# Performance work log

Measured on AMD Instinct MI355X. Metric: run time of the kernel, lower is better.

## Reference

```python
import jax, jax.numpy as jnp
import numpy as np

NEG_BIG = -9.0e15  # matches torch's -9000000000000000.0
LEAKY_SLOPE = 0.01  # nn.LeakyReLU default


def setup_inputs() -> dict:
    key = jax.random.key(0)
    k1, k2, k3, k4, k5, k6 = jax.random.split(key, 6)
    B, N, NEMB, NHID = 1, 8192, 128, 64
    x = jax.random.normal(k1, (B, N, NEMB), dtype=jnp.float32)
    adj = jax.random.randint(k2, (B, N, N), 0, 2, dtype=jnp.int32)
    # learned parameters (xavier-ish scale)
    w_weight = jax.random.normal(k3, (NHID, NEMB), dtype=jnp.float32) * (1.0 / np.sqrt(NEMB))
    w_bias = jnp.zeros((NHID,), dtype=jnp.float32)
    a_weight = jax.random.normal(k4, (1, 2 * NHID), dtype=jnp.float32) * (1.0 / np.sqrt(2 * NHID))
    a_bias = jnp.zeros((1,), dtype=jnp.float32)
    return {"x": x, "adj": adj, "w_weight": w_weight, "w_bias": w_bias,
            "a_weight": a_weight, "a_bias": a_bias}


def reference(x, adj, w_weight, w_bias, a_weight, a_bias):
    # h = W x + b : [B, N, F]
    h = jnp.einsum("bnd,fd->bnf", x, w_weight) + w_bias
    F = h.shape[-1]
    # The torch code forms a[b,i,j] = concat(h_i, h_j) then Linear(2F->1).
    # Equivalent decomposition avoids the [B,N,N,2F] tensor:
    # e[b,i,j] = leaky_relu(h_i . a_src + h_j . a_dst + a_bias)
    a_src, a_dst = a_weight[0, :F], a_weight[0, F:]
    s_src = jnp.einsum("bnf,f->bn", h, a_src)  # [B, N]
    s_dst = jnp.einsum("bnf,f->bn", h, a_dst)  # [B, N]
    e = jax.nn.leaky_relu(s_src[:, :, None] + s_dst[:, None, :] + a_bias[0],
                          negative_slope=LEAKY_SLOPE)  # [B, N, N]
    # masked_scatter_ semantics: True positions (row-major over the WHOLE
    # flattened tensor) receive e's elements taken sequentially in order.
    mask_flat = (adj > 0).reshape(-1)
    take_idx = jnp.cumsum(mask_flat.astype(jnp.int32)) - 1  # position in source stream
    src_flat = e.reshape(-1)
    att = jnp.where(mask_flat, src_flat[take_idx], jnp.float32(NEG_BIG)).reshape(e.shape)
    # softmax over dim=2, dropout in eval mode (identity)
    att = jax.nn.softmax(att, axis=2)
    out = jax.nn.elu(jnp.einsum("bij,bjf->bif", att, h))  # [B, N, F]
    return out
```

## Files before the change

kernel.cpp:

```cpp
#include <hip/hip_runtime.h>
#include <hip/hip_bf16.h>
#include <cstdint>
#include <cstddef>

#define N 8192
#define F 64
#define NEMB 128
#define BI 16
#define BJ 256
#define NWRD (N/16)
#define LEAKY 0.01f

typedef __attribute__((ext_vector_type(8))) short bf16x8;
typedef __attribute__((ext_vector_type(4))) float f32x4;

__device__ __forceinline__ float wave_reduce_sum_f(float v){
  #pragma unroll
  for (int d = 32; d > 0; d >>= 1) v += __shfl_xor(v, d, 64);
  return v;
}
__device__ __forceinline__ int wave_reduce_sum_i(int v){
  #pragma unroll
  for (int d = 32; d > 0; d >>= 1) v += __shfl_xor(v, d, 64);
  return v;
}
__device__ __forceinline__ int wave_incl_scan_i(int v, int lane){
  #pragma unroll
  for (int d = 1; d < 64; d <<= 1){
    int u = __shfl_up(v, d, 64);
    if (lane >= d) v += u;
  }
  return v;
}
__device__ __forceinline__ unsigned short f2bf(float x){
  union { float f; unsigned u; } v; v.f = x;
  unsigned r = v.u + 0x7fff + ((v.u >> 16) & 1);
  return (unsigned short)(r >> 16);
}

extern "C" __global__ void __launch_bounds__(256)
k_h(const float* __restrict__ x, const float* __restrict__ ww, const float* __restrict__ wb,
    const float* __restrict__ aw, float* __restrict__ h,
    float* __restrict__ ssrc, float* __restrict__ sdst){
  __shared__ float xs[4][NEMB];
  const int t = threadIdx.x, w = t >> 6, lane = t & 63;
  const int n0 = blockIdx.x * 4;
  ((float2*)&xs[0][0])[t] = ((const float2*)(x + (size_t)n0 * NEMB))[t];
  __syncthreads();
  const int n = n0 + w;
  const float4* w4 = (const float4*)(ww + (size_t)lane * NEMB);
  const float4* x4 = (const float4*)&xs[w][0];
  float acc = wb[lane];
  #pragma unroll
  for (int k = 0; k < NEMB/4; ++k){
    float4 a = x4[k]; float4 b = w4[k];
    acc = fmaf(a.x, b.x, acc);
    acc = fmaf(a.y, b.y, acc);
    acc = fmaf(a.z, b.z, acc);
    acc = fmaf(a.w, b.w, acc);
  }
  h[(size_t)n * F + lane] = acc;
  float vs = wave_reduce_sum_f(acc * aw[lane]);
  float vd = wave_reduce_sum_f(acc * aw[F + lane]);
  if (lane == 0){ ssrc[n] = vs; sdst[n] = vd; }
}

extern "C" __global__ void __launch_bounds__(256)
k_tr(const float* __restrict__ h, unsigned short* __restrict__ ht){
  __shared__ float tile[64][65];
  const int t = threadIdx.x;
  const int n0 = blockIdx.x * 64;
  #pragma unroll
  for (int s = 0; s < 4; ++s){
    const int r = s*16 + (t>>4);
    const int c = (t&15)*4;
    const float4 v = *(const float4*)(h + (size_t)(n0+r)*F + c);
    tile[r][c] = v.x; tile[r][c+1] = v.y; tile[r][c+2] = v.z; tile[r][c+3] = v.w;
  }
  __syncthreads();
  const int f = t >> 2, jq = t & 3;
  unsigned short buf[16];
  #pragma unroll
  for (int k = 0; k < 16; ++k) buf[k] = f2bf(tile[jq*16 + k][f]);
  *(uint4*)(ht + (size_t)f*N + n0 + jq*16)     = *(uint4*)&buf[0];
  *(uint4*)(ht + (size_t)f*N + n0 + jq*16 + 8) = *(uint4*)&buf[8];
}

extern "C" __global__ void __launch_bounds__(256)
k_pack(const int* __restrict__ adj, unsigned short* __restrict__ bm, int* __restrict__ cnt){
  const int i = blockIdx.x, t = threadIdx.x;
  int total = 0;
  #pragma unroll
  for (int half = 0; half < 2; ++half){
    const int jb = half*4096 + t*16;
    const int4* p4 = (const int4*)(adj + (size_t)i*N + jb);
    unsigned m = 0;
    #pragma unroll
    for (int k = 0; k < 4; ++k){
      int4 a = p4[k];
      m |= (unsigned)(a.x > 0) << (k*4+0);
      m |= (unsigned)(a.y > 0) << (k*4+1);
      m |= (unsigned)(a.z > 0) << (k*4+2);
      m |= (unsigned)(a.w > 0) << (k*4+3);
    }
    bm[(size_t)i*NWRD + (jb>>4)] = (unsigned short)m;
    total += __popc(m);
  }
  total = wave_reduce_sum_i(total);
  __shared__ int ws_[4];
  if ((t & 63) == 0) ws_[t >> 6] = total;
  __syncthreads();
  if (t == 0) cnt[i] = ws_[0] + ws_[1] + ws_[2] + ws_[3];
}

extern "C" __global__ void __launch_bounds__(1024)
k_scan(const int* __restrict__ cnt, int* __restrict__ base){
  __shared__ int wsum[16];
  const int t = threadIdx.x, lane = t & 63, w = t >> 6;
  int4 aa = ((const int4*)cnt)[t * 2];
  int4 bb = ((const int4*)cnt)[t * 2 + 1];
  int v[8] = {aa.x, aa.y, aa.z, aa.w, bb.x, bb.y, bb.z, bb.w};
  int local = 0;
  #pragma unroll
  for (int k = 0; k < 8; ++k){ int tmp = v[k]; v[k] = local; local += tmp; }
  int inc = wave_incl_scan_i(local, lane);
  int wexcl = inc - local;
  if (lane == 63) wsum[w] = inc;
  __syncthreads();
  if (t == 0){
    int run = 0;
    #pragma unroll
    for (int k = 0; k < 16; ++k){ int tmp = wsum[k]; wsum[k] = run; run += tmp; }
  }
  __syncthreads();
  const int b0 = wsum[w] + wexcl;
  ((int4*)base)[t * 2]     = make_int4(b0 + v[0], b0 + v[1], b0 + v[2], b0 + v[3]);
  ((int4*)base)[t * 2 + 1] = make_int4(b0 + v[4], b0 + v[5], b0 + v[6], b0 + v[7]);
}

extern "C" __global__ void __launch_bounds__(256, 3)
k_main(const unsigned short* __restrict__ bm, const unsigned short* __restrict__ ht,
       const float* __restrict__ ssrc, const float* __restrict__ sdst,
       const float* __restrict__ abias, const int* __restrict__ base,
       float* __restrict__ out){
  __shared__ __attribute__((aligned(16))) char ht_lds[64*512];
  __shared__ __attribute__((aligned(16))) char pt_lds[16*512];
  __shared__ float denom_lds[BI];
  const int t = threadIdx.x, w = t >> 6, lane = t & 63;
  const int i0 = blockIdx.x * BI;
  const int r = t >> 4, g = t & 15;
  const float ab = abias[0];
  int rank = base[i0 + r];
  float dsum = 0.f;
  f32x4 acc = {0.f, 0.f, 0.f, 0.f};

  const int fr = lane & 15, ks = lane >> 4;
  const int fB = w*16 + fr;
  const char* aBase = pt_lds + fr*512;
  const char* bBase = ht_lds + fB*512;
  const int sA = (fr & 7) << 4;
  const int sB = (fB & 7) << 4;

  for (int j0 = 0; j0 < N; j0 += BJ){
    __syncthreads();
    #pragma unroll
    for (int k = 0; k < 8; ++k){
      const int L = (w*8 + k) * 1024;
      const int f = (w*8 + k) * 2 + (lane >> 5);
      const int b = (lane & 31) * 16;
      const char* src = (const char*)ht + (size_t)f*(N*2) + j0*2 + (b ^ ((f & 7) << 4));
      __builtin_amdgcn_global_load_lds((const __attribute__((address_space(1))) void*)src,
                                       (__attribute__((address_space(3))) void*)(ht_lds + L),
                                       16, 0, 0);
    }
    {
      const unsigned m = bm[(size_t)(i0 + r)*NWRD + (j0 >> 4) + g];
      const int c = __popc(m);
      int inc = c;
      #pragma unroll
      for (int d = 1; d < 16; d <<= 1){
        int u = __shfl_up(inc, d, 16);
        if (g >= d) inc += u;
      }
      const int rowtot = __shfl(inc, 15, 16);
      int q = rank + inc - c;
      rank += rowtot;
      unsigned pk[8];
      #pragma unroll
      for (int bb = 0; bb < 16; ++bb){
        float p = 0.f;
        if ((m >> bb) & 1u){
          float e = ssrc[q >> 13] + sdst[q & (N - 1)] + ab;
          e = (e > 0.f) ? e : LEAKY * e;
          p = __expf(e);
          dsum += p;
          ++q;
        }
        if (bb & 1) pk[bb >> 1] |= (unsigned)f2bf(p) << 16;
        else        pk[bb >> 1]  = (unsigned)f2bf(p);
      }
      char* pb = pt_lds + r*512;
      const int sw = (r & 7) << 4;
      *(uint4*)(pb + ((g*32)      ^ sw)) = make_uint4(pk[0], pk[1], pk[2], pk[3]);
      *(uint4*)(pb + ((g*32 + 16) ^ sw)) = make_uint4(pk[4], pk[5], pk[6], pk[7]);
    }
    __syncthreads();
    #pragma unroll
    for (int kk = 0; kk < 8; ++kk){
      const int off = kk*64 + ks*16;
      bf16x8 av = *(const bf16x8*)(aBase + (off ^ sA));
      bf16x8 bv = *(const bf16x8*)(bBase + (off ^ sB));
      acc = __builtin_amdgcn_mfma_f32_16x16x32_bf16(av, bv, acc, 0, 0, 0);
    }
  }
  #pragma unroll
  for (int d = 8; d > 0; d >>= 1) dsum += __shfl_xor(dsum, d, 16);
  if (g == 0) denom_lds[r] = dsum;
  __syncthreads();
  #pragma unroll
  for (int reg = 0; reg < 4; ++reg){
    const int il = ks*4 + reg;
    const float dn = denom_lds[il];
    float v = (dn > 0.f) ? acc[reg] / dn : 0.f;
    const float o = (v > 0.f) ? v : (__expf(v) - 1.f);
    out[(size_t)(i0 + il)*F + w*16 + fr] = o;
  }
}

extern "C" void kernel_launch(void* const* d_in, const int* in_sizes, int n_in,
                              void* d_out, int out_size, void* d_ws, size_t ws_size,
                              hipStream_t stream){
  const float* x   = (const float*)d_in[0];
  const int*   adj = (const int*)d_in[1];
  const float* ww  = (const float*)d_in[2];
  const float* wb  = (const float*)d_in[3];
  const float* aw  = (const float*)d_in[4];
  const float* ab  = (const float*)d_in[5];
  float* out = (float*)d_out;

  char* ws = (char*)d_ws;
  float*          h    = (float*)(ws);
  unsigned short* ht   = (unsigned short*)(ws + (size_t)N*F*4);
  float*          ssrc = (float*)(ws + (size_t)N*F*4 + (size_t)N*F*2);
  float*          sdst = ssrc + N;
  int*            cnt  = (int*)(sdst + N);
  int*            base = cnt + N;
  unsigned short* bm   = (unsigned short*)(base + N);

  k_h   <<<N/4,  256, 0, stream>>>(x, ww, wb, aw, h, ssrc, sdst);
  k_tr  <<<N/64, 256, 0, stream>>>(h, ht);
  k_pack<<<N,    256, 0, stream>>>(adj, bm, cnt);
  k_scan<<<1,   1024, 0, stream>>>(cnt, base);
  k_main<<<N/BI, 256, 0, stream>>>(bm, ht, ssrc, sdst, ab, base, out);
}
```

Baseline: 187.5 us.

## Fuse adjacency packing and prefix scan into main kernel via decoupled lookback

Removes the separate pack and scan kernels. Each main block now takes a dynamic ticket, packs its 16 adjacency rows into an LDS bitmask, and computes its global rank offset with a single-pass decoupled-lookback scan over per-block partials. The per-bit rank inside the inner loop is now computed with popcount instead of a serial increment. This cuts two launches and the round trip of the bitmask through global memory. In exchange LDS use rises, the occupancy hint drops from 3 to 2 blocks, and blocks serialize on the lookback spin.

```diff
diff --git a/kernel.cpp b/kernel.cpp
--- a/kernel.cpp
+++ b/kernel.cpp
@@ -8,7 +8,7 @@
 #define NEMB 128
 #define BI 16
 #define BJ 256
-#define NWRD (N/16)
+#define NBLK (N/BI)
 #define LEAKY 0.01f
 
 typedef __attribute__((ext_vector_type(8))) short bf16x8;
@@ -22,14 +22,6 @@
 __device__ __forceinline__ int wave_reduce_sum_i(int v){
   #pragma unroll
   for (int d = 32; d > 0; d >>= 1) v += __shfl_xor(v, d, 64);
-  return v;
-}
-__device__ __forceinline__ int wave_incl_scan_i(int v, int lane){
-  #pragma unroll
-  for (int d = 1; d < 64; d <<= 1){
-    int u = __shfl_up(v, d, 64);
-    if (lane >= d) v += u;
-  }
   return v;
 }
 __device__ __forceinline__ unsigned short f2bf(float x){
@@ -41,9 +33,14 @@
 extern "C" __global__ void __launch_bounds__(256)
 k_h(const float* __restrict__ x, const float* __restrict__ ww, const float* __restrict__ wb,
     const float* __restrict__ aw, float* __restrict__ h,
-    float* __restrict__ ssrc, float* __restrict__ sdst){
+    float* __restrict__ ssrc, float* __restrict__ sdst,
+    unsigned* __restrict__ partials, int* __restrict__ ticket){
+  const int t = threadIdx.x, w = t >> 6, lane = t & 63;
+  if (blockIdx.x == 0){
+    partials[t] = 0; partials[t + 256] = 0;
+    if (t == 0) *ticket = 0;
+  }
   __shared__ float xs[4][NEMB];
-  const int t = threadIdx.x, w = t >> 6, lane = t & 63;
   const int n0 = blockIdx.x * 4;
   ((float2*)&xs[0][0])[t] = ((const float2*)(x + (size_t)n0 * NEMB))[t];
   __syncthreads();
@@ -86,71 +83,76 @@
   *(uint4*)(ht + (size_t)f*N + n0 + jq*16 + 8) = *(uint4*)&buf[8];
 }
 
-extern "C" __global__ void __launch_bounds__(256)
-k_pack(const int* __restrict__ adj, unsigned short* __restrict__ bm, int* __restrict__ cnt){
-  const int i = blockIdx.x, t = threadIdx.x;
-  int total = 0;
-  #pragma unroll
-  for (int half = 0; half < 2; ++half){
-    const int jb = half*4096 + t*16;
-    const int4* p4 = (const int4*)(adj + (size_t)i*N + jb);
-    unsigned m = 0;
-    #pragma unroll
-    for (int k = 0; k < 4; ++k){
-      int4 a = p4[k];
-      m |= (unsigned)(a.x > 0) << (k*4+0);
-      m |= (unsigned)(a.y > 0) << (k*4+1);
-      m |= (unsigned)(a.z > 0) << (k*4+2);
-      m |= (unsigned)(a.w > 0) << (k*4+3);
-    }
-    bm[(size_t)i*NWRD + (jb>>4)] = (unsigned short)m;
-    total += __popc(m);
-  }
-  total = wave_reduce_sum_i(total);
-  __shared__ int ws_[4];
-  if ((t & 63) == 0) ws_[t >> 6] = total;
-  __syncthreads();
-  if (t == 0) cnt[i] = ws_[0] + ws_[1] + ws_[2] + ws_[3];
-}
-
-extern "C" __global__ void __launch_bounds__(1024)
-k_scan(const int* __restrict__ cnt, int* __restrict__ base){
-  __shared__ int wsum[16];
-  const int t = threadIdx.x, lane = t & 63, w = t >> 6;
-  int4 aa = ((const int4*)cnt)[t * 2];
-  int4 bb = ((const int4*)cnt)[t * 2 + 1];
-  int v[8] = {aa.x, aa.y, aa.z, aa.w, bb.x, bb.y, bb.z, bb.w};
-  int local = 0;
-  #pragma unroll
-  for (int k = 0; k < 8; ++k){ int tmp = v[k]; v[k] = local; local += tmp; }
-  int inc = wave_incl_scan_i(local, lane);
-  int wexcl = inc - local;
-  if (lane == 63) wsum[w] = inc;
-  __syncthreads();
+extern "C" __global__ void __launch_bounds__(256, 2)
+k_main(const int* __restrict__ adj, const unsigned short* __restrict__ ht,
+       const float* __restrict__ ssrc, const float* __restrict__ sdst,
+       const float* __restrict__ abias,
+       unsigned* __restrict__ partials, int* __restrict__ ticket,
+       float* __restrict__ out){
+  __shared__ __attribute__((aligned(16))) char ht_lds[64*512];
+  __shared__ __attribute__((aligned(16))) char pt_lds[16*512];
+  __shared__ unsigned short bm_lds[BI][N/16];
+  __shared__ float denom_lds[BI];
+  __shared__ int cnt_lds[BI];
+  __shared__ int base_lds[BI];
+  __shared__ int vid_s, gbase_s;
+
+  const int t = threadIdx.x, w = t >> 6, lane = t & 63;
+  if (t == 0) vid_s = atomicAdd(ticket, 1);
+  __syncthreads();
+  const int vid = vid_s;
+  const int i0 = vid * BI;
+
+  #pragma unroll
+  for (int rr = 0; rr < 4; ++rr){
+    const int i = i0 + w*4 + rr;
+    const int4* row4 = (const int4*)(adj + (size_t)i * N);
+    int rcnt = 0;
+    #pragma unroll 4
+    for (int it = 0; it < 32; ++it){
+      const int4 a = row4[it*64 + lane];
+      unsigned nib = (unsigned)(a.x>0) | ((unsigned)(a.y>0)<<1) |
+                     ((unsigned)(a.z>0)<<2) | ((unsigned)(a.w>0)<<3);
+      rcnt += __popc(nib);
+      unsigned word = nib << ((lane & 3) * 4);
+      word |= __shfl_xor(word, 1, 64);
+      word |= __shfl_xor(word, 2, 64);
+      if ((lane & 3) == 0) bm_lds[w*4+rr][it*16 + (lane>>2)] = (unsigned short)word;
+    }
+    rcnt = wave_reduce_sum_i(rcnt);
+    if (lane == 0) cnt_lds[w*4+rr] = rcnt;
+  }
+  __syncthreads();
+
   if (t == 0){
     int run = 0;
     #pragma unroll
-    for (int k = 0; k < 16; ++k){ int tmp = wsum[k]; wsum[k] = run; run += tmp; }
-  }
-  __syncthreads();
-  const int b0 = wsum[w] + wexcl;
-  ((int4*)base)[t * 2]     = make_int4(b0 + v[0], b0 + v[1], b0 + v[2], b0 + v[3]);
-  ((int4*)base)[t * 2 + 1] = make_int4(b0 + v[4], b0 + v[5], b0 + v[6], b0 + v[7]);
-}
-
-extern "C" __global__ void __launch_bounds__(256, 3)
-k_main(const unsigned short* __restrict__ bm, const unsigned short* __restrict__ ht,
-       const float* __restrict__ ssrc, const float* __restrict__ sdst,
-       const float* __restrict__ abias, const int* __restrict__ base,
-       float* __restrict__ out){
-  __shared__ __attribute__((aligned(16))) char ht_lds[64*512];
-  __shared__ __attribute__((aligned(16))) char pt_lds[16*512];
-  __shared__ float denom_lds[BI];
-  const int t = threadIdx.x, w = t >> 6, lane = t & 63;
-  const int i0 = blockIdx.x * BI;
+    for (int k = 0; k < BI; ++k){ int c = cnt_lds[k]; base_lds[k] = run; run += c; }
+    const unsigned pub = ((unsigned)run << 2) | (vid == 0 ? 2u : 1u);
+    __hip_atomic_store(&partials[vid], pub, __ATOMIC_RELEASE, __HIP_MEMORY_SCOPE_AGENT);
+    unsigned long long excl = 0;
+    if (vid > 0){
+      int look = vid - 1;
+      while (1){
+        unsigned v;
+        do {
+          v = __hip_atomic_load(&partials[look], __ATOMIC_ACQUIRE, __HIP_MEMORY_SCOPE_AGENT);
+        } while (!(v & 3u));
+        excl += (v >> 2);
+        if ((v & 3u) == 2u) break;
+        --look;
+      }
+      __hip_atomic_store(&partials[vid],
+                         (unsigned)(((excl + (unsigned long long)(unsigned)run) << 2) | 2u),
+                         __ATOMIC_RELEASE, __HIP_MEMORY_SCOPE_AGENT);
+    }
+    gbase_s = (int)excl;
+  }
+  __syncthreads();
+
   const int r = t >> 4, g = t & 15;
   const float ab = abias[0];
-  int rank = base[i0 + r];
+  int rank = gbase_s + base_lds[r];
   float dsum = 0.f;
   f32x4 acc = {0.f, 0.f, 0.f, 0.f};
 
@@ -174,7 +176,7 @@
                                        16, 0, 0);
     }
     {
-      const unsigned m = bm[(size_t)(i0 + r)*NWRD + (j0 >> 4) + g];
+      const unsigned m = bm_lds[r][(j0 >> 4) + g];
       const int c = __popc(m);
       int inc = c;
       #pragma unroll
@@ -183,18 +185,18 @@
         if (g >= d) inc += u;
       }
       const int rowtot = __shfl(inc, 15, 16);
-      int q = rank + inc - c;
+      const int q0 = rank + inc - c;
       rank += rowtot;
       unsigned pk[8];
       #pragma unroll
       for (int bb = 0; bb < 16; ++bb){
         float p = 0.f;
         if ((m >> bb) & 1u){
-          float e = ssrc[q >> 13] + sdst[q & (N - 1)] + ab;
+          const int qb = q0 + __popc(m & ((1u << bb) - 1u));
+          float e = ssrc[qb >> 13] + sdst[qb & (N - 1)] + ab;
           e = (e > 0.f) ? e : LEAKY * e;
           p = __expf(e);
           dsum += p;
-          ++q;
         }
         if (bb & 1) pk[bb >> 1] |= (unsigned)f2bf(p) << 16;
         else        pk[bb >> 1]  = (unsigned)f2bf(p);
@@ -239,17 +241,14 @@
   float* out = (float*)d_out;
 
   char* ws = (char*)d_ws;
-  float*          h    = (float*)(ws);
-  unsigned short* ht   = (unsigned short*)(ws + (size_t)N*F*4);
-  float*          ssrc = (float*)(ws + (size_t)N*F*4 + (size_t)N*F*2);
-  float*          sdst = ssrc + N;
-  int*            cnt  = (int*)(sdst + N);
-  int*            base = cnt + N;
-  unsigned short* bm   = (unsigned short*)(base + N);
-
-  k_h   <<<N/4,  256, 0, stream>>>(x, ww, wb, aw, h, ssrc, sdst);
+  float*          h        = (float*)(ws);
+  unsigned short* ht       = (unsigned short*)(ws + (size_t)N*F*4);
+  float*          ssrc     = (float*)(ws + (size_t)N*F*4 + (size_t)N*F*2);
+  float*          sdst     = ssrc + N;
+  unsigned*       partials = (unsigned*)(sdst + N);
+  int*            ticket   = (int*)(partials + NBLK);
+
+  k_h   <<<N/4,  256, 0, stream>>>(x, ww, wb, aw, h, ssrc, sdst, partials, ticket);
   k_tr  <<<N/64, 256, 0, stream>>>(h, ht);
-  k_pack<<<N,    256, 0, stream>>>(adj, bm, cnt);
-  k_scan<<<1,   1024, 0, stream>>>(cnt, base);
-  k_main<<<N/BI, 256, 0, stream>>>(bm, ht, ssrc, sdst, ab, base, out);
-}
+  k_main<<<NBLK, 256, 0, stream>>>(adj, ht, ssrc, sdst, ab, partials, ticket, out);
+}
```

After: 360.5 us. 1.92x slower.

## Split attention rows across two blocks, double-buffer P tiles, and stream sdst contiguously

Applied to the files above, without the earlier changes.

The main kernel now splits each 16-row group's j-range into two halves handled by separate blocks, which write partial numerators and denominators that a new combine kernel reduces before applying ELU. P tiles are double-buffered in LDS with a single barrier per chunk. The h^T operand is read straight from global into registers instead of staged through LDS. The masked-scatter gather now reads a contiguous 16-wide window of a duplicated sdst array and picks the matching ssrc per element, replacing scattered per-bit loads, and the bitmask is stored chunk-major with per-chunk popcounts. This adds more blocks and occupancy in exchange for extra partial-sum traffic and an additional kernel launch.

```diff
diff --git a/kernel.cpp b/kernel.cpp
--- a/kernel.cpp
+++ b/kernel.cpp
@@ -1,5 +1,4 @@
 #include <hip/hip_runtime.h>
-#include <hip/hip_bf16.h>
 #include <cstdint>
 #include <cstddef>
 
@@ -8,7 +7,8 @@
 #define NEMB 128
 #define BI 16
 #define BJ 256
-#define NWRD (N/16)
+#define NCHUNK 32
+#define HALFCH 16
 #define LEAKY 0.01f
 
 typedef __attribute__((ext_vector_type(8))) short bf16x8;
@@ -41,9 +41,9 @@
 extern "C" __global__ void __launch_bounds__(256)
 k_h(const float* __restrict__ x, const float* __restrict__ ww, const float* __restrict__ wb,
     const float* __restrict__ aw, float* __restrict__ h,
-    float* __restrict__ ssrc, float* __restrict__ sdst){
+    float* __restrict__ ssrc, float* __restrict__ sdst2x){
+  const int t = threadIdx.x, w = t >> 6, lane = t & 63;
   __shared__ float xs[4][NEMB];
-  const int t = threadIdx.x, w = t >> 6, lane = t & 63;
   const int n0 = blockIdx.x * 4;
   ((float2*)&xs[0][0])[t] = ((const float2*)(x + (size_t)n0 * NEMB))[t];
   __syncthreads();
@@ -62,7 +62,7 @@
   h[(size_t)n * F + lane] = acc;
   float vs = wave_reduce_sum_f(acc * aw[lane]);
   float vd = wave_reduce_sum_f(acc * aw[F + lane]);
-  if (lane == 0){ ssrc[n] = vs; sdst[n] = vd; }
+  if (lane == 0){ ssrc[n] = vs; sdst2x[n] = vd; sdst2x[n + N] = vd; }
 }
 
 extern "C" __global__ void __launch_bounds__(256)
@@ -87,30 +87,38 @@
 }
 
 extern "C" __global__ void __launch_bounds__(256)
-k_pack(const int* __restrict__ adj, unsigned short* __restrict__ bm, int* __restrict__ cnt){
+k_pack(const int* __restrict__ adj, unsigned short* __restrict__ bm,
+       unsigned short* __restrict__ ccnt, int* __restrict__ rowtot){
   const int i = blockIdx.x, t = threadIdx.x;
   int total = 0;
   #pragma unroll
   for (int half = 0; half < 2; ++half){
-    const int jb = half*4096 + t*16;
-    const int4* p4 = (const int4*)(adj + (size_t)i*N + jb);
+    const int w = half*256 + t;
+    const int4* p4 = (const int4*)(adj + (size_t)i*N + w*16);
     unsigned m = 0;
     #pragma unroll
     for (int k = 0; k < 4; ++k){
       int4 a = p4[k];
-      m |= (unsigned)(a.x > 0) << (k*4+0);
-      m |= (unsigned)(a.y > 0) << (k*4+1);
-      m |= (unsigned)(a.z > 0) << (k*4+2);
-      m |= (unsigned)(a.w > 0) << (k*4+3);
+      m |= (unsigned)(a.x>0) << (k*4+0);
+      m |= (unsigned)(a.y>0) << (k*4+1);
+      m |= (unsigned)(a.z>0) << (k*4+2);
+      m |= (unsigned)(a.w>0) << (k*4+3);
     }
-    bm[(size_t)i*NWRD + (jb>>4)] = (unsigned short)m;
-    total += __popc(m);
+    bm[((size_t)(w>>4)*N + i)*16 + (w&15)] = (unsigned short)m;
+    const int pc = __popc(m);
+    total += pc;
+    int cs = pc;
+    cs += __shfl_xor(cs, 1, 16);
+    cs += __shfl_xor(cs, 2, 16);
+    cs += __shfl_xor(cs, 4, 16);
+    cs += __shfl_xor(cs, 8, 16);
+    if ((t & 15) == 0) ccnt[(size_t)i*NCHUNK + (w>>4)] = (unsigned short)cs;
   }
   total = wave_reduce_sum_i(total);
   __shared__ int ws_[4];
   if ((t & 63) == 0) ws_[t >> 6] = total;
   __syncthreads();
-  if (t == 0) cnt[i] = ws_[0] + ws_[1] + ws_[2] + ws_[3];
+  if (t == 0) rowtot[i] = ws_[0] + ws_[1] + ws_[2] + ws_[3];
 }
 
 extern "C" __global__ void __launch_bounds__(1024)
@@ -138,93 +146,141 @@
   ((int4*)base)[t * 2 + 1] = make_int4(b0 + v[4], b0 + v[5], b0 + v[6], b0 + v[7]);
 }
 
-extern "C" __global__ void __launch_bounds__(256, 3)
-k_main(const unsigned short* __restrict__ bm, const unsigned short* __restrict__ ht,
-       const float* __restrict__ ssrc, const float* __restrict__ sdst,
-       const float* __restrict__ abias, const int* __restrict__ base,
-       float* __restrict__ out){
-  __shared__ __attribute__((aligned(16))) char ht_lds[64*512];
-  __shared__ __attribute__((aligned(16))) char pt_lds[16*512];
-  __shared__ float denom_lds[BI];
+extern "C" __global__ void __launch_bounds__(256, 4)
+k_main(const unsigned short* __restrict__ bm, const unsigned short* __restrict__ ccnt,
+       const int* __restrict__ base, const unsigned short* __restrict__ ht,
+       const float* __restrict__ ssrc, const float* __restrict__ sdst2x,
+       const float* __restrict__ abias,
+       float* __restrict__ pnum, float* __restrict__ pden){
+  __shared__ __attribute__((aligned(16))) char pt[2][16*512];
+  __shared__ unsigned short ccum[BI][HALFCH];
+  __shared__ int basel[BI];
+
   const int t = threadIdx.x, w = t >> 6, lane = t & 63;
-  const int i0 = blockIdx.x * BI;
+  const int vid = blockIdx.x >> 1, half = blockIdx.x & 1;
+  const int i0 = vid * BI;
+  const int ch0 = half * HALFCH;
+
+  if (t < BI) basel[t] = base[i0 + t];
+  {
+    const int r = t >> 4, g = t & 15;
+    int c = (int)ccnt[(size_t)(i0+r)*NCHUNK + ch0 + g];
+    int pre = 0;
+    if (half){
+      pre = (int)ccnt[(size_t)(i0+r)*NCHUNK + g];
+      #pragma unroll
+      for (int d = 1; d < 16; d <<= 1) pre += __shfl_xor(pre, d, 16);
+    }
+    int inc = c;
+    #pragma unroll
+    for (int d = 1; d < 16; d <<= 1){ int u = __shfl_up(inc, d, 16); if (g >= d) inc += u; }
+    ccum[r][g] = (unsigned short)(pre + inc - c);
+  }
+  __syncthreads();
+
   const int r = t >> 4, g = t & 15;
+  const int fr = lane & 15, ks = lane >> 4;
+  const int fB = w*16 + fr;
+  char* buf0 = pt[0];
+  char* buf1 = pt[1];
+  const int sA = (fr & 7) << 4;
+  const int sw = (r & 7) << 4;
   const float ab = abias[0];
-  int rank = base[i0 + r];
+  const int rowbase = basel[r];
   float dsum = 0.f;
   f32x4 acc = {0.f, 0.f, 0.f, 0.f};
-
-  const int fr = lane & 15, ks = lane >> 4;
-  const int fB = w*16 + fr;
-  const char* aBase = pt_lds + fr*512;
-  const char* bBase = ht_lds + fB*512;
-  const int sA = (fr & 7) << 4;
-  const int sB = (fB & 7) << 4;
-
-  for (int j0 = 0; j0 < N; j0 += BJ){
+  bf16x8 bregA[8], bregB[8];
+
+#define PREFETCH(CH, BR) { \
+    const unsigned short* hBp = ht + (size_t)fB*N + (CH)*BJ + ks*8; \
+    _Pragma("unroll") \
+    for (int kk = 0; kk < 8; ++kk) BR[kk] = *(const bf16x8*)(hBp + kk*32); \
+  }
+
+#define PRODUCE(CC, PB) { \
+    const int cc_ = (CC); \
+    const int ch = ch0 + cc_; \
+    const unsigned m = (unsigned)bm[((size_t)ch*N + (i0+r))*16 + g]; \
+    const int c = __popc(m); \
+    int inc = c; \
+    _Pragma("unroll") \
+    for (int d = 1; d < 16; d <<= 1){ int u = __shfl_up(inc, d, 16); if (g >= d) inc += u; } \
+    const int qex = inc - c; \
+    const int q0row = rowbase + (int)ccum[r][cc_]; \
+    const float* sdw = sdst2x + (q0row & (N - 1)) + qex; \
+    const int ilo = q0row >> 13; \
+    const float s_lo = ssrc[ilo]; \
+    const float s_hi = ssrc[ilo + 1]; \
+    const int krel = ((ilo + 1) << 13) - q0row - qex; \
+    char* myreg = (PB) + r*512; \
+    *(uint4*)(myreg + ((g*32)      ^ sw)) = make_uint4(0,0,0,0); \
+    *(uint4*)(myreg + ((g*32 + 16) ^ sw)) = make_uint4(0,0,0,0); \
+    float wv[16]; \
+    _Pragma("unroll") \
+    for (int k = 0; k < 16; ++k) wv[k] = sdw[k]; \
+    unsigned mc = m; \
+    _Pragma("unroll") \
+    for (int k = 0; k < 16; ++k){ \
+      const float ss = (k >= krel) ? s_hi : s_lo; \
+      float e = ss + wv[k] + ab; \
+      e = (e > 0.f) ? e : LEAKY * e; \
+      const float p = __expf(e); \
+      const int pos = __ffs(mc) - 1; \
+      if (k < c){ \
+        dsum += p; \
+        *(unsigned short*)(myreg + ((g*32 + pos*2) ^ sw)) = f2bf(p); \
+      } \
+      mc &= mc - 1; \
+    } \
+  }
+
+#define MM(PB, BR) { \
+    const char* aP = (PB) + fr*512; \
+    _Pragma("unroll") \
+    for (int kk = 0; kk < 8; ++kk){ \
+      bf16x8 av = *(const bf16x8*)(aP + ((kk*64 + ks*16) ^ sA)); \
+      acc = __builtin_amdgcn_mfma_f32_16x16x32_bf16(av, BR[kk], acc, 0, 0, 0); \
+    } \
+  }
+
+  PREFETCH(ch0, bregA)
+  PRODUCE(0, buf0)
+  __syncthreads();
+  for (int cc = 0; cc < HALFCH; cc += 2){
+    PREFETCH(ch0 + cc + 1, bregB)
+    PRODUCE(cc + 1, buf1)
+    MM(buf0, bregA)
     __syncthreads();
-    #pragma unroll
-    for (int k = 0; k < 8; ++k){
-      const int L = (w*8 + k) * 1024;
-      const int f = (w*8 + k) * 2 + (lane >> 5);
-      const int b = (lane & 31) * 16;
-      const char* src = (const char*)ht + (size_t)f*(N*2) + j0*2 + (b ^ ((f & 7) << 4));
-      __builtin_amdgcn_global_load_lds((const __attribute__((address_space(1))) void*)src,
-                                       (__attribute__((address_space(3))) void*)(ht_lds + L),
-                                       16, 0, 0);
+    if (cc + 2 < HALFCH){
+      PREFETCH(ch0 + cc + 2, bregA)
+      PRODUCE(cc + 2, buf0)
     }
-    {
-      const unsigned m = bm[(size_t)(i0 + r)*NWRD + (j0 >> 4) + g];
-      const int c = __popc(m);
-      int inc = c;
-      #pragma unroll
-      for (int d = 1; d < 16; d <<= 1){
-        int u = __shfl_up(inc, d, 16);
-        if (g >= d) inc += u;
-      }
-      const int rowtot = __shfl(inc, 15, 16);
-      int q = rank + inc - c;
-      rank += rowtot;
-      unsigned pk[8];
-      #pragma unroll
-      for (int bb = 0; bb < 16; ++bb){
-        float p = 0.f;
-        if ((m >> bb) & 1u){
-          float e = ssrc[q >> 13] + sdst[q & (N - 1)] + ab;
-          e = (e > 0.f) ? e : LEAKY * e;
-          p = __expf(e);
-          dsum += p;
-          ++q;
-        }
-        if (bb & 1) pk[bb >> 1] |= (unsigned)f2bf(p) << 16;
-        else        pk[bb >> 1]  = (unsigned)f2bf(p);
-      }
-      char* pb = pt_lds + r*512;
-      const int sw = (r & 7) << 4;
-      *(uint4*)(pb + ((g*32)      ^ sw)) = make_uint4(pk[0], pk[1], pk[2], pk[3]);
-      *(uint4*)(pb + ((g*32 + 16) ^ sw)) = make_uint4(pk[4], pk[5], pk[6], pk[7]);
-    }
+    MM(buf1, bregB)
     __syncthreads();
-    #pragma unroll
-    for (int kk = 0; kk < 8; ++kk){
-      const int off = kk*64 + ks*16;
-      bf16x8 av = *(const bf16x8*)(aBase + (off ^ sA));
-      bf16x8 bv = *(const bf16x8*)(bBase + (off ^ sB));
-      acc = __builtin_amdgcn_mfma_f32_16x16x32_bf16(av, bv, acc, 0, 0, 0);
-    }
-  }
+  }
+#undef PREFETCH
+#undef PRODUCE
+#undef MM
+
   #pragma unroll
   for (int d = 8; d > 0; d >>= 1) dsum += __shfl_xor(dsum, d, 16);
-  if (g == 0) denom_lds[r] = dsum;
-  __syncthreads();
+  if (g == 0) pden[(size_t)half*N + i0 + r] = dsum;
   #pragma unroll
   for (int reg = 0; reg < 4; ++reg){
     const int il = ks*4 + reg;
-    const float dn = denom_lds[il];
-    float v = (dn > 0.f) ? acc[reg] / dn : 0.f;
-    const float o = (v > 0.f) ? v : (__expf(v) - 1.f);
-    out[(size_t)(i0 + il)*F + w*16 + fr] = o;
-  }
+    pnum[(size_t)half*N*F + (size_t)(i0 + il)*F + fB] = acc[reg];
+  }
+}
+
+extern "C" __global__ void __launch_bounds__(256)
+k_comb(const float* __restrict__ pnum, const float* __restrict__ pden,
+       float* __restrict__ out){
+  const int idx = blockIdx.x * 256 + threadIdx.x;
+  const int i = idx >> 6;
+  const float dn = pden[i] + pden[N + i];
+  const float nm = pnum[idx] + pnum[(size_t)N*F + idx];
+  float v = (dn > 0.f) ? nm / dn : 0.f;
+  out[idx] = (v > 0.f) ? v : (__expf(v) - 1.f);
 }
 
 extern "C" void kernel_launch(void* const* d_in, const int* in_sizes, int n_in,
@@ -239,17 +295,21 @@
   float* out = (float*)d_out;
 
   char* ws = (char*)d_ws;
-  float*          h    = (float*)(ws);
-  unsigned short* ht   = (unsigned short*)(ws + (size_t)N*F*4);
-  float*          ssrc = (float*)(ws + (size_t)N*F*4 + (size_t)N*F*2);
-  float*          sdst = ssrc + N;
-  int*            cnt  = (int*)(sdst + N);
-  int*            base = cnt + N;
-  unsigned short* bm   = (unsigned short*)(base + N);
-
-  k_h   <<<N/4,  256, 0, stream>>>(x, ww, wb, aw, h, ssrc, sdst);
-  k_tr  <<<N/64, 256, 0, stream>>>(h, ht);
-  k_pack<<<N,    256, 0, stream>>>(adj, bm, cnt);
-  k_scan<<<1,   1024, 0, stream>>>(cnt, base);
-  k_main<<<N/BI, 256, 0, stream>>>(bm, ht, ssrc, sdst, ab, base, out);
-}
+  float*          h      = (float*)(ws);
+  unsigned short* ht     = (unsigned short*)(ws + (2u<<20));
+  float*          ssrc   = (float*)(ws + (3u<<20));
+  float*          sdst2x = (float*)(ws + (3u<<20) + 32*1024);
+  int*            rowtot = (int*)(ws + (3u<<20) + 96*1024);
+  int*            base   = (int*)(ws + (3u<<20) + 128*1024);
+  unsigned short* ccnt   = (unsigned short*)(ws + (3u<<20) + 160*1024);
+  unsigned short* bm     = (unsigned short*)(ws + (4u<<20));
+  float*          pnum   = (float*)(ws + (12u<<20));
+  float*          pden   = (float*)(ws + (16u<<20));
+
+  k_pack<<<N,      256, 0, stream>>>(adj, bm, ccnt, rowtot);
+  k_h   <<<N/4,    256, 0, stream>>>(x, ww, wb, aw, h, ssrc, sdst2x);
+  k_tr  <<<N/64,   256, 0, stream>>>(h, ht);
+  k_scan<<<1,     1024, 0, stream>>>(rowtot, base);
+  k_main<<<2*(N/BI), 256, 0, stream>>>(bm, ccnt, base, ht, ssrc, sdst2x, ab, pnum, pden);
+  k_comb<<<(N*F)/256, 256, 0, stream>>>(pnum, pden, out);
+}
```

New measurement: 169.3 us. -9.7%, faster.
